# Optimization experiments

Measured on AMD Instinct MI355X. Metric: run time of the kernel, lower is better.

Reference implementation:

```python
import jax, jax.numpy as jnp
import numpy as np

D_MODEL = 1024
N_HEADS = 16
D_FF = 4096
HEAD_DIM = D_MODEL // N_HEADS
EPS = 1e-5


def setup_inputs() -> dict:
    key = jax.random.key(0)
    ks = jax.random.split(key, 12)
    B, S, D = 2, 2048, D_MODEL
    s = 0.02
    return {
        "x": jax.random.normal(ks[0], (B, S, D), jnp.float32),
        "ln1_g": jnp.ones((D,), jnp.float32),
        "ln1_b": jnp.zeros((D,), jnp.float32),
        "qkv_w": jax.random.normal(ks[1], (3 * D, D), jnp.float32) * s,
        "qkv_b": jnp.zeros((3 * D,), jnp.float32),
        "out_w": jax.random.normal(ks[2], (D, D), jnp.float32) * s,
        "out_b": jnp.zeros((D,), jnp.float32),
        "ln2_g": jnp.ones((D,), jnp.float32),
        "ln2_b": jnp.zeros((D,), jnp.float32),
        "fc1_w": jax.random.normal(ks[3], (D_FF, D), jnp.float32) * s,
        "fc1_b": jnp.zeros((D_FF,), jnp.float32),
        "fc2_w": jax.random.normal(ks[4], (D, D_FF), jnp.float32) * s,
        "fc2_b": jnp.zeros((D,), jnp.float32),
    }


def _layernorm(x, g, b):
    mu = jnp.mean(x, axis=-1, keepdims=True)
    var = jnp.mean(jnp.square(x - mu), axis=-1, keepdims=True)
    return (x - mu) * jax.lax.rsqrt(var + EPS) * g + b


def _attention(h, qkv_w, qkv_b, out_w, out_b):
    B, S, D = h.shape
    qkv = h @ qkv_w.T + qkv_b  # [B,S,3D]
    q, k, v = jnp.split(qkv, 3, axis=-1)
    # [B,H,S,hd]
    q = q.reshape(B, S, N_HEADS, HEAD_DIM).transpose(0, 2, 1, 3)
    k = k.reshape(B, S, N_HEADS, HEAD_DIM).transpose(0, 2, 1, 3)
    v = v.reshape(B, S, N_HEADS, HEAD_DIM).transpose(0, 2, 1, 3)
    scale = HEAD_DIM ** -0.5
    scores = jnp.einsum("bhqd,bhkd->bhqk", q, k) * scale
    causal = jnp.tril(jnp.ones((S, S), bool))
    scores = jnp.where(causal, scores, -jnp.inf)
    attn = jax.nn.softmax(scores, axis=-1)
    out = jnp.einsum("bhqk,bhkd->bhqd", attn, v)
    out = out.transpose(0, 2, 1, 3).reshape(B, S, D)
    return out @ out_w.T + out_b


def reference(x, ln1_g, ln1_b, qkv_w, qkv_b, out_w, out_b,
              ln2_g, ln2_b, fc1_w, fc1_b, fc2_w, fc2_b):
    x = x + _attention(_layernorm(x, ln1_g, ln1_b), qkv_w, qkv_b, out_w, out_b)
    h = _layernorm(x, ln2_g, ln2_b)
    ff = jax.nn.gelu(h @ fc1_w.T + fc1_b, approximate=False) @ fc2_w.T + fc2_b
    return x + ff
```

## Files before the change

### kernel.cpp

```cpp
#include <hip/hip_runtime.h>
#include <stdint.h>

typedef uint16_t u16;
typedef uint32_t u32;
typedef __bf16 bf16_t;
typedef bf16_t bf16x8 __attribute__((ext_vector_type(8)));
typedef float f32x4 __attribute__((ext_vector_type(4)));
typedef u16 u16x4 __attribute__((ext_vector_type(4)));
typedef u16 u16x8 __attribute__((ext_vector_type(8)));

__device__ __forceinline__ float bf2f(u16 v) {
    union { u32 u; float f; } x; x.u = ((u32)v) << 16; return x.f;
}
__device__ __forceinline__ u16 f2bf(float f) {
    union { float f; u32 u; } x; x.f = f;
    u32 r = (x.u + 0x7fffu + ((x.u >> 16) & 1u)) >> 16;
    return (u16)r;
}

__device__ __forceinline__ void gload_lds16(const u16* g, u16* l) {
    __builtin_amdgcn_global_load_lds(
        (const __attribute__((address_space(1))) void*)g,
        (__attribute__((address_space(3))) void*)l,
        16, 0, 0);
}
#define WAIT_ALL() __builtin_amdgcn_s_waitcnt(0)
#define WAITVM(n) __builtin_amdgcn_s_waitcnt(0x0F70 | (n))
#define BARRIER() __builtin_amdgcn_s_barrier()

__global__ __launch_bounds__(256) void cvt_kernel(
    const float* __restrict__ src, u16* __restrict__ dst, int n4)
{
    int i = blockIdx.x * 256 + threadIdx.x;
    if (i >= n4) return;
    f32x4 v = ((const f32x4*)src)[i];
    u16x4 o;
#pragma unroll
    for (int j = 0; j < 4; j++) o[j] = f2bf(v[j]);
    ((u16x4*)dst)[i] = o;
}

__global__ __launch_bounds__(256) void ln_kernel(
    const float* __restrict__ x, const float* __restrict__ g,
    const float* __restrict__ b, u16* __restrict__ out)
{
    const int row = blockIdx.x;
    const int tid = threadIdx.x;
    f32x4 xv = *(const f32x4*)(x + (size_t)row * 1024 + tid * 4);
    float v[4];
    float s = 0.f, s2 = 0.f;
#pragma unroll
    for (int i = 0; i < 4; i++) { v[i] = xv[i]; s += v[i]; s2 += v[i] * v[i]; }
#pragma unroll
    for (int off = 1; off < 64; off <<= 1) {
        s  += __shfl_xor(s, off);
        s2 += __shfl_xor(s2, off);
    }
    __shared__ float ws1[4], ws2[4];
    if ((tid & 63) == 0) { ws1[tid >> 6] = s; ws2[tid >> 6] = s2; }
    __syncthreads();
    s  = ws1[0] + ws1[1] + ws1[2] + ws1[3];
    s2 = ws2[0] + ws2[1] + ws2[2] + ws2[3];
    float mu  = s * (1.0f / 1024.0f);
    float var = s2 * (1.0f / 1024.0f) - mu * mu;
    float rstd = rsqrtf(var + 1e-5f);
    f32x4 gv = *(const f32x4*)(g + tid * 4);
    f32x4 bv = *(const f32x4*)(b + tid * 4);
    u16x4 ov;
#pragma unroll
    for (int i = 0; i < 4; i++)
        ov[i] = f2bf((v[i] - mu) * rstd * gv[i] + bv[i]);
    *(u16x4*)(out + (size_t)row * 1024 + tid * 4) = ov;
}

__global__ __launch_bounds__(256, 2) void gemm_bt(
    const u16* __restrict__ A, const u16* __restrict__ Bt,
    const float* __restrict__ bias, const float* res,
    void* C, int N, int K, int lda, int gelu)
{
    __shared__ __align__(16) u16 sA[2][128 * 32];
    __shared__ __align__(16) u16 sB[2][128 * 32];
    const int tid  = threadIdx.x;
    const int wave = tid >> 6, lane = tid & 63;
    const int lm = lane & 15, quad = lane >> 4;
    const int wm = wave >> 1, wn = wave & 1;
    const int row0 = blockIdx.y * 128, col0 = blockIdx.x * 128;
    const int r16 = lane >> 2;
    const int c8  = (lane & 3) * 8;
    const int niter = K >> 5;

    const u16* gsrc;
    size_t gstride;
    int chunk0;
    if (wave < 2) {
        chunk0 = wave * 4;
        gsrc = A + (size_t)(row0 + chunk0 * 16 + r16) * lda + c8;
        gstride = lda;
    } else {
        chunk0 = (wave - 2) * 4;
        gsrc = Bt + (size_t)(col0 + chunk0 * 16 + r16) * K + c8;
        gstride = K;
    }
    u16* lbase0 = (wave < 2) ? &sA[0][chunk0 * 512] : &sB[0][chunk0 * 512];
    u16* lbase1 = (wave < 2) ? &sA[1][chunk0 * 512] : &sB[1][chunk0 * 512];

    f32x4 acc[4][4];
#pragma unroll
    for (int i = 0; i < 4; i++)
#pragma unroll
        for (int j = 0; j < 4; j++) acc[i][j] = f32x4{0.f, 0.f, 0.f, 0.f};

#pragma unroll
    for (int j = 0; j < 4; j++)
        gload_lds16(gsrc + (size_t)(j * 16) * gstride, lbase0 + j * 512);

    for (int k = 0; k < niter; k++) {
        const int cur = k & 1;
        if (k + 1 < niter) {
            const u16* gs = gsrc + (size_t)(k + 1) * 32;
            u16* lb = cur ? lbase0 : lbase1;
#pragma unroll
            for (int j = 0; j < 4; j++)
                gload_lds16(gs + (size_t)(j * 16) * gstride, lb + j * 512);
            WAITVM(4);
        } else {
            WAITVM(0);
        }
        BARRIER();

        bf16x8 af[4], bfr[4];
#pragma unroll
        for (int t = 0; t < 4; t++)
            af[t] = *(const bf16x8*)&sA[cur][(wm * 64 + t * 16 + lm) * 32 + quad * 8];
#pragma unroll
        for (int t = 0; t < 4; t++)
            bfr[t] = *(const bf16x8*)&sB[cur][(wn * 64 + t * 16 + lm) * 32 + quad * 8];
#pragma unroll
        for (int i = 0; i < 4; i++)
#pragma unroll
            for (int j = 0; j < 4; j++)
                acc[i][j] = __builtin_amdgcn_mfma_f32_16x16x32_bf16(af[i], bfr[j], acc[i][j], 0, 0, 0);

        BARRIER();
    }

    float bj[4];
#pragma unroll
    for (int j = 0; j < 4; j++) bj[j] = bias[col0 + wn * 64 + j * 16 + lm];
#pragma unroll
    for (int i = 0; i < 4; i++) {
        int rbase = row0 + wm * 64 + i * 16 + quad * 4;
#pragma unroll
        for (int j = 0; j < 4; j++) {
            int c = col0 + wn * 64 + j * 16 + lm;
#pragma unroll
            for (int r = 0; r < 4; r++) {
                float v = acc[i][j][r] + bj[j];
                if (gelu) v = 0.5f * v * (1.0f + erff(v * 0.70710678118f));
                size_t idx = (size_t)(rbase + r) * N + c;
                if (res) {
                    ((float*)C)[idx] = v + res[idx];
                } else {
                    ((u16*)C)[idx] = f2bf(v);
                }
            }
        }
    }
}

__global__ __launch_bounds__(256, 2) void gemm_bt64(
    const u16* __restrict__ A, const u16* __restrict__ Bt,
    const float* __restrict__ bias, const float* res,
    void* C, int N, int K, int lda, int gelu)
{
    __shared__ __align__(16) u16 sA[2][128 * 32];
    __shared__ __align__(16) u16 sB[2][64 * 32];
    const int tid  = threadIdx.x;
    const int wave = tid >> 6, lane = tid & 63;
    const int lm = lane & 15, quad = lane >> 4;
    const int wm = wave >> 1, wn = wave & 1;
    const int row0 = blockIdx.y * 128, col0 = blockIdx.x * 64;
    const int r16 = lane >> 2;
    const int c8  = (lane & 3) * 8;
    const int niter = K >> 5;

    const u16* gs_[3];
    u16* lb0_[3];
    u16* lb1_[3];
    size_t gstride_[3];
#pragma unroll
    for (int j = 0; j < 3; j++) {
        int cid = wave * 3 + j;
        if (cid < 8) {
            gs_[j] = A + (size_t)(row0 + cid * 16 + r16) * lda + c8;
            gstride_[j] = lda;
            lb0_[j] = &sA[0][cid * 512];
            lb1_[j] = &sA[1][cid * 512];
        } else {
            int bc = cid - 8;
            gs_[j] = Bt + (size_t)(col0 + bc * 16 + r16) * K + c8;
            gstride_[j] = K;
            lb0_[j] = &sB[0][bc * 512];
            lb1_[j] = &sB[1][bc * 512];
        }
    }

    f32x4 acc[4][2];
#pragma unroll
    for (int i = 0; i < 4; i++)
#pragma unroll
        for (int j = 0; j < 2; j++) acc[i][j] = f32x4{0.f, 0.f, 0.f, 0.f};

#pragma unroll
    for (int j = 0; j < 3; j++) gload_lds16(gs_[j], lb0_[j]);

    for (int k = 0; k < niter; k++) {
        const int cur = k & 1;
        if (k + 1 < niter) {
#pragma unroll
            for (int j = 0; j < 3; j++)
                gload_lds16(gs_[j] + (size_t)(k + 1) * 32, cur ? lb0_[j] : lb1_[j]);
            WAITVM(3);
        } else {
            WAITVM(0);
        }
        BARRIER();

        bf16x8 af[4], bfr[2];
#pragma unroll
        for (int t = 0; t < 4; t++)
            af[t] = *(const bf16x8*)&sA[cur][(wm * 64 + t * 16 + lm) * 32 + quad * 8];
#pragma unroll
        for (int t = 0; t < 2; t++)
            bfr[t] = *(const bf16x8*)&sB[cur][(wn * 32 + t * 16 + lm) * 32 + quad * 8];
#pragma unroll
        for (int i = 0; i < 4; i++)
#pragma unroll
            for (int j = 0; j < 2; j++)
                acc[i][j] = __builtin_amdgcn_mfma_f32_16x16x32_bf16(af[i], bfr[j], acc[i][j], 0, 0, 0);

        BARRIER();
    }

    float bj[2];
#pragma unroll
    for (int j = 0; j < 2; j++) bj[j] = bias[col0 + wn * 32 + j * 16 + lm];
#pragma unroll
    for (int i = 0; i < 4; i++) {
        int rbase = row0 + wm * 64 + i * 16 + quad * 4;
#pragma unroll
        for (int j = 0; j < 2; j++) {
            int c = col0 + wn * 32 + j * 16 + lm;
#pragma unroll
            for (int r = 0; r < 4; r++) {
                float v = acc[i][j][r] + bj[j];
                if (gelu) v = 0.5f * v * (1.0f + erff(v * 0.70710678118f));
                size_t idx = (size_t)(rbase + r) * N + c;
                if (res) {
                    ((float*)C)[idx] = v + res[idx];
                } else {
                    ((u16*)C)[idx] = f2bf(v);
                }
            }
        }
    }
}

__global__ __launch_bounds__(256, 4) void attn_kernel(u16* qkv)
{
    __shared__ __align__(16) u16 sQ[64 * 64];
    __shared__ __align__(16) u16 sK[64 * 64];
    __shared__ __align__(16) u16 sVT[64 * 64];
    __shared__ __align__(16) u16 sP[4 * 16 * 72];

    const int tid  = threadIdx.x;
    const int wave = tid >> 6, lane = tid & 63;
    const int lm = lane & 15, quad = lane >> 4;
    int xi = blockIdx.x;
    int qz = (xi & 1) ? (31 - (xi >> 1)) : (xi >> 1);
    int qi = ((blockIdx.y >> 3) & 1) ? (31 - qz) : qz;
    const int q0 = qi * 64;
    const int b = blockIdx.y >> 4, h = blockIdx.y & 15;
    const size_t tok0 = (size_t)b * 2048;
    const int qcol = h * 64, kcol = 1024 + h * 64, vcol = 2048 + h * 64;
    const int r8 = lane >> 3;
    const int c8 = (lane & 7) * 8;

#pragma unroll
    for (int j = 0; j < 2; j++) {
        int chunk = wave * 2 + j;
        int r = chunk * 8 + r8;
        gload_lds16(qkv + (tok0 + q0 + r) * 3072 + qcol + c8, &sQ[chunk * 512]);
    }
    WAIT_ALL();
    __syncthreads();

    bf16x8 aq[2];
#pragma unroll
    for (int kk = 0; kk < 2; kk++)
        aq[kk] = *(const bf16x8*)&sQ[(wave * 16 + lm) * 64 + kk * 32 + quad * 8];

    f32x4 oacc[4];
    float mrun[4], lrun[4];
#pragma unroll
    for (int n = 0; n < 4; n++) oacc[n] = f32x4{0.f, 0.f, 0.f, 0.f};
#pragma unroll
    for (int r = 0; r < 4; r++) { mrun[r] = -1e30f; lrun[r] = 0.f; }

    const int vkey = tid >> 2;
    const int vdq  = (tid & 3) * 16;
    const int vpos = (((vkey >> 3) ^ (tid & 3)) << 3) | (vkey & 7);

    u16* sPw = &sP[wave * 16 * 72];
    const int ntiles = qi + 1;

    for (int tk = 0; tk < ntiles; tk++) {
        const int kb = tk * 64;
        __syncthreads();
#pragma unroll
        for (int j = 0; j < 2; j++) {
            int chunk = wave * 2 + j;
            int r = chunk * 8 + r8;
            gload_lds16(qkv + (tok0 + kb + r) * 3072 + kcol + c8, &sK[chunk * 512]);
        }
        {
            const u16* vr = qkv + (tok0 + kb + vkey) * 3072 + vcol + vdq;
            u16x8 v0 = *(const u16x8*)vr;
            u16x8 v1 = *(const u16x8*)(vr + 8);
#pragma unroll
            for (int i = 0; i < 8; i++) sVT[(vdq + i) * 64 + vpos] = v0[i];
#pragma unroll
            for (int i = 0; i < 8; i++) sVT[(vdq + 8 + i) * 64 + vpos] = v1[i];
        }
        WAIT_ALL();
        __syncthreads();

        float sc[4][4];
#pragma unroll
        for (int n = 0; n < 4; n++) {
            f32x4 s = f32x4{0.f, 0.f, 0.f, 0.f};
#pragma unroll
            for (int kk = 0; kk < 2; kk++) {
                bf16x8 bk = *(const bf16x8*)&sK[(n * 16 + lm) * 64 + kk * 32 + quad * 8];
                s = __builtin_amdgcn_mfma_f32_16x16x32_bf16(aq[kk], bk, s, 0, 0, 0);
            }
            int col  = kb + n * 16 + lm;
            int rowb = q0 + wave * 16 + quad * 4;
#pragma unroll
            for (int r = 0; r < 4; r++)
                sc[n][r] = (col <= rowb + r) ? s[r] * 0.125f : -1e30f;
        }
#pragma unroll
        for (int r = 0; r < 4; r++) {
            float mx = fmaxf(fmaxf(sc[0][r], sc[1][r]), fmaxf(sc[2][r], sc[3][r]));
#pragma unroll
            for (int off = 1; off < 16; off <<= 1) mx = fmaxf(mx, __shfl_xor(mx, off));
            float mnew  = fmaxf(mrun[r], mx);
            float alpha = __expf(mrun[r] - mnew);
            float sum = 0.f;
#pragma unroll
            for (int n = 0; n < 4; n++) {
                float p = __expf(sc[n][r] - mnew);
                sc[n][r] = p;
                sum += p;
            }
#pragma unroll
            for (int off = 1; off < 16; off <<= 1) sum += __shfl_xor(sum, off);
            lrun[r] = lrun[r] * alpha + sum;
            mrun[r] = mnew;
#pragma unroll
            for (int n = 0; n < 4; n++) oacc[n][r] *= alpha;
        }
#pragma unroll
        for (int n = 0; n < 4; n++)
#pragma unroll
            for (int r = 0; r < 4; r++)
                sPw[(quad * 4 + r) * 72 + n * 16 + lm] = f2bf(sc[n][r]);
        bf16x8 ap[2];
#pragma unroll
        for (int kk = 0; kk < 2; kk++)
            ap[kk] = *(const bf16x8*)&sPw[lm * 72 + kk * 32 + quad * 8];
#pragma unroll
        for (int n = 0; n < 4; n++)
#pragma unroll
            for (int kk = 0; kk < 2; kk++) {
                bf16x8 bv = *(const bf16x8*)
                    &sVT[(n * 16 + lm) * 64 + (((kk * 4 + quad) ^ n) << 3)];
                oacc[n] = __builtin_amdgcn_mfma_f32_16x16x32_bf16(ap[kk], bv, oacc[n], 0, 0, 0);
            }
    }

    {
        int rowb = q0 + wave * 16 + quad * 4;
#pragma unroll
        for (int r = 0; r < 4; r++) {
            float inv = 1.0f / lrun[r];
#pragma unroll
            for (int n = 0; n < 4; n++) {
                int d = n * 16 + lm;
                qkv[(tok0 + rowb + r) * 3072 + qcol + d] = f2bf(oacc[n][r] * inv);
            }
        }
    }
}

extern "C" void kernel_launch(void* const* d_in, const int* in_sizes, int n_in,
                              void* d_out, int out_size, void* d_ws, size_t ws_size,
                              hipStream_t stream)
{
    (void)in_sizes; (void)n_in; (void)out_size; (void)ws_size;
    const float* x    = (const float*)d_in[0];
    const float* ln1g = (const float*)d_in[1];
    const float* ln1b = (const float*)d_in[2];
    const float* qkvwF= (const float*)d_in[3];
    const float* qkvb = (const float*)d_in[4];
    const float* outwF= (const float*)d_in[5];
    const float* outb = (const float*)d_in[6];
    const float* ln2g = (const float*)d_in[7];
    const float* ln2b = (const float*)d_in[8];
    const float* fc1wF= (const float*)d_in[9];
    const float* fc1b = (const float*)d_in[10];
    const float* fc2wF= (const float*)d_in[11];
    const float* fc2b = (const float*)d_in[12];
    float* out = (float*)d_out;
    u16*   ws  = (u16*)d_ws;
    const int M1 = 1 << 20;

    u16* qkvw = ws;
    u16* outw = ws + 3 * M1;
    u16* qkvB = ws + 4 * M1;
    u16* ff1  = ws;
    u16* fc1w = ws + 16 * M1;
    u16* fc2w = ws + 20 * M1;
    u16* h    = ws + 24 * M1;

    cvt_kernel<<<3072, 256, 0, stream>>>(qkvwF, qkvw, 3 * M1 / 4);
    cvt_kernel<<<1024, 256, 0, stream>>>(outwF, outw, 1 * M1 / 4);
    cvt_kernel<<<4096, 256, 0, stream>>>(fc1wF, fc1w, 4 * M1 / 4);
    cvt_kernel<<<4096, 256, 0, stream>>>(fc2wF, fc2w, 4 * M1 / 4);

    ln_kernel<<<4096, 256, 0, stream>>>(x, ln1g, ln1b, h);
    gemm_bt<<<dim3(24, 32), 256, 0, stream>>>(h, qkvw, qkvb, nullptr, qkvB,
                                              3072, 1024, 1024, 0);
    attn_kernel<<<dim3(32, 32), 256, 0, stream>>>(qkvB);
    gemm_bt64<<<dim3(16, 32), 256, 0, stream>>>(qkvB, outw, outb, x, out,
                                                1024, 1024, 3072, 0);
    ln_kernel<<<4096, 256, 0, stream>>>(out, ln2g, ln2b, h);
    gemm_bt<<<dim3(32, 32), 256, 0, stream>>>(h, fc1w, fc1b, nullptr, ff1,
                                              4096, 1024, 1024, 1);
    gemm_bt64<<<dim3(16, 32), 256, 0, stream>>>(ff1, fc2w, fc2b, out, out,
                                                1024, 4096, 4096, 0);
}
```

Before: 401.8 us.

## Double-buffer K/V tiles in attention, swizzle LDS, merge weight conversions

The attention kernel now double-buffers K and transposed-V tiles in LDS, prefetching the next tile's K via async global-to-LDS loads and V into registers while the current tile is computed. Q/K/V LDS layouts get an XOR swizzle to reduce bank conflicts. The four weight-conversion launches are merged into a single kernel to cut launch overhead. The doubled LDS footprint lowers the occupancy hint from 4 to 3 blocks per CU, and the loop adds an extra barrier per tile.

```diff
diff --git a/kernel.cpp b/kernel.cpp
--- a/kernel.cpp
+++ b/kernel.cpp
@@ -26,18 +26,26 @@
 }
 #define WAIT_ALL() __builtin_amdgcn_s_waitcnt(0)
 #define WAITVM(n) __builtin_amdgcn_s_waitcnt(0x0F70 | (n))
+#define WAIT_LGKM0() __builtin_amdgcn_s_waitcnt(0xC07F)
 #define BARRIER() __builtin_amdgcn_s_barrier()
 
-__global__ __launch_bounds__(256) void cvt_kernel(
-    const float* __restrict__ src, u16* __restrict__ dst, int n4)
+__global__ __launch_bounds__(256) void cvt4_kernel(
+    const float* __restrict__ s0, const float* __restrict__ s1,
+    const float* __restrict__ s2, const float* __restrict__ s3,
+    u16* __restrict__ d0, u16* __restrict__ d1,
+    u16* __restrict__ d2, u16* __restrict__ d3)
 {
     int i = blockIdx.x * 256 + threadIdx.x;
-    if (i >= n4) return;
-    f32x4 v = ((const f32x4*)src)[i];
+    const float* s; u16* d; int off;
+    if (i < 786432)       { s = s0; d = d0; off = i; }
+    else if (i < 1048576) { s = s1; d = d1; off = i - 786432; }
+    else if (i < 2097152) { s = s2; d = d2; off = i - 1048576; }
+    else                  { s = s3; d = d3; off = i - 2097152; }
+    f32x4 v = ((const f32x4*)s)[off];
     u16x4 o;
 #pragma unroll
     for (int j = 0; j < 4; j++) o[j] = f2bf(v[j]);
-    ((u16x4*)dst)[i] = o;
+    ((u16x4*)d)[off] = o;
 }
 
 __global__ __launch_bounds__(256) void ln_kernel(
@@ -187,23 +195,22 @@
     const u16* gs_[3];
     u16* lb0_[3];
     u16* lb1_[3];
-    size_t gstride_[3];
 #pragma unroll
     for (int j = 0; j < 3; j++) {
         int cid = wave * 3 + j;
         if (cid < 8) {
             gs_[j] = A + (size_t)(row0 + cid * 16 + r16) * lda + c8;
-            gstride_[j] = lda;
             lb0_[j] = &sA[0][cid * 512];
             lb1_[j] = &sA[1][cid * 512];
         } else {
             int bc = cid - 8;
             gs_[j] = Bt + (size_t)(col0 + bc * 16 + r16) * K + c8;
-            gstride_[j] = K;
             lb0_[j] = &sB[0][bc * 512];
             lb1_[j] = &sB[1][bc * 512];
         }
     }
+    const size_t gstride_a = lda, gstride_b = K;
+    (void)gstride_a; (void)gstride_b;
 
     f32x4 acc[4][2];
 #pragma unroll
@@ -266,11 +273,11 @@
     }
 }
 
-__global__ __launch_bounds__(256, 4) void attn_kernel(u16* qkv)
+__global__ __launch_bounds__(256, 3) void attn_kernel(u16* qkv)
 {
     __shared__ __align__(16) u16 sQ[64 * 64];
-    __shared__ __align__(16) u16 sK[64 * 64];
-    __shared__ __align__(16) u16 sVT[64 * 64];
+    __shared__ __align__(16) u16 sK[2][64 * 64];
+    __shared__ __align__(16) u16 sVT[2][64 * 64];
     __shared__ __align__(16) u16 sP[4 * 16 * 72];
 
     const int tid  = threadIdx.x;
@@ -284,21 +291,35 @@
     const size_t tok0 = (size_t)b * 2048;
     const int qcol = h * 64, kcol = 1024 + h * 64, vcol = 2048 + h * 64;
     const int r8 = lane >> 3;
-    const int c8 = (lane & 7) * 8;
+    const int c8s = (((lane & 7) ^ r8) << 3);
+
+    const int vkey = tid >> 2;
+    const int vq   = tid & 3;
+    const int vdq  = vq * 16;
+    const u16* vbase = qkv + (tok0 + vkey) * 3072 + vcol + vdq;
 
 #pragma unroll
     for (int j = 0; j < 2; j++) {
         int chunk = wave * 2 + j;
         int r = chunk * 8 + r8;
-        gload_lds16(qkv + (tok0 + q0 + r) * 3072 + qcol + c8, &sQ[chunk * 512]);
-    }
-    WAIT_ALL();
-    __syncthreads();
+        gload_lds16(qkv + (tok0 + q0 + r) * 3072 + qcol + c8s, &sQ[chunk * 512]);
+    }
+#pragma unroll
+    for (int j = 0; j < 2; j++) {
+        int chunk = wave * 2 + j;
+        int r = chunk * 8 + r8;
+        gload_lds16(qkv + (tok0 + r) * 3072 + kcol + c8s, &sK[0][chunk * 512]);
+    }
+    u16x8 va = *(const u16x8*)vbase;
+    u16x8 vb = *(const u16x8*)(vbase + 8);
+    WAITVM(4);
+    BARRIER();
 
     bf16x8 aq[2];
 #pragma unroll
     for (int kk = 0; kk < 2; kk++)
-        aq[kk] = *(const bf16x8*)&sQ[(wave * 16 + lm) * 64 + kk * 32 + quad * 8];
+        aq[kk] = *(const bf16x8*)
+            &sQ[(wave * 16 + lm) * 64 + (((kk * 4 + quad) ^ (lm & 7)) << 3)];
 
     f32x4 oacc[4];
     float mrun[4], lrun[4];
@@ -307,41 +328,51 @@
 #pragma unroll
     for (int r = 0; r < 4; r++) { mrun[r] = -1e30f; lrun[r] = 0.f; }
 
-    const int vkey = tid >> 2;
-    const int vdq  = (tid & 3) * 16;
-    const int vpos = (((vkey >> 3) ^ (tid & 3)) << 3) | (vkey & 7);
-
     u16* sPw = &sP[wave * 16 * 72];
     const int ntiles = qi + 1;
 
     for (int tk = 0; tk < ntiles; tk++) {
+        const int cur = tk & 1;
+        u16x8 na = va, nb = vb;
+        if (tk + 1 < ntiles) {
+            const int kb1 = (tk + 1) * 64;
+#pragma unroll
+            for (int j = 0; j < 2; j++) {
+                int chunk = wave * 2 + j;
+                int r = chunk * 8 + r8;
+                gload_lds16(qkv + (tok0 + kb1 + r) * 3072 + kcol + c8s,
+                            &sK[1 - cur][chunk * 512]);
+            }
+            const u16* vr = vbase + (size_t)kb1 * 3072;
+            na = *(const u16x8*)vr;
+            nb = *(const u16x8*)(vr + 8);
+            WAITVM(4);
+        } else {
+            WAITVM(0);
+        }
+#pragma unroll
+        for (int i = 0; i < 8; i++) {
+            int d = vdq + i;
+            sVT[cur][d * 64 + ((((vkey >> 3) ^ i ^ vq)) << 3) + (vkey & 7)] = va[i];
+        }
+#pragma unroll
+        for (int i = 0; i < 8; i++) {
+            int d = vdq + 8 + i;
+            sVT[cur][d * 64 + ((((vkey >> 3) ^ i ^ vq)) << 3) + (vkey & 7)] = vb[i];
+        }
+        va = na; vb = nb;
+        WAIT_LGKM0();
+        BARRIER();
+
         const int kb = tk * 64;
-        __syncthreads();
-#pragma unroll
-        for (int j = 0; j < 2; j++) {
-            int chunk = wave * 2 + j;
-            int r = chunk * 8 + r8;
-            gload_lds16(qkv + (tok0 + kb + r) * 3072 + kcol + c8, &sK[chunk * 512]);
-        }
-        {
-            const u16* vr = qkv + (tok0 + kb + vkey) * 3072 + vcol + vdq;
-            u16x8 v0 = *(const u16x8*)vr;
-            u16x8 v1 = *(const u16x8*)(vr + 8);
-#pragma unroll
-            for (int i = 0; i < 8; i++) sVT[(vdq + i) * 64 + vpos] = v0[i];
-#pragma unroll
-            for (int i = 0; i < 8; i++) sVT[(vdq + 8 + i) * 64 + vpos] = v1[i];
-        }
-        WAIT_ALL();
-        __syncthreads();
-
         float sc[4][4];
 #pragma unroll
         for (int n = 0; n < 4; n++) {
             f32x4 s = f32x4{0.f, 0.f, 0.f, 0.f};
 #pragma unroll
             for (int kk = 0; kk < 2; kk++) {
-                bf16x8 bk = *(const bf16x8*)&sK[(n * 16 + lm) * 64 + kk * 32 + quad * 8];
+                bf16x8 bk = *(const bf16x8*)
+                    &sK[cur][(n * 16 + lm) * 64 + (((kk * 4 + quad) ^ (lm & 7)) << 3)];
                 s = __builtin_amdgcn_mfma_f32_16x16x32_bf16(aq[kk], bk, s, 0, 0, 0);
             }
             int col  = kb + n * 16 + lm;
@@ -385,9 +416,12 @@
 #pragma unroll
             for (int kk = 0; kk < 2; kk++) {
                 bf16x8 bv = *(const bf16x8*)
-                    &sVT[(n * 16 + lm) * 64 + (((kk * 4 + quad) ^ n) << 3)];
+                    &sVT[cur][(n * 16 + lm) * 64 +
+                              ((((kk * 4 + quad) ^ (lm & 7) ^ n)) << 3)];
                 oacc[n] = __builtin_amdgcn_mfma_f32_16x16x32_bf16(ap[kk], bv, oacc[n], 0, 0, 0);
             }
+
+        BARRIER();
     }
 
     {
@@ -434,10 +468,8 @@
     u16* fc2w = ws + 20 * M1;
     u16* h    = ws + 24 * M1;
 
-    cvt_kernel<<<3072, 256, 0, stream>>>(qkvwF, qkvw, 3 * M1 / 4);
-    cvt_kernel<<<1024, 256, 0, stream>>>(outwF, outw, 1 * M1 / 4);
-    cvt_kernel<<<4096, 256, 0, stream>>>(fc1wF, fc1w, 4 * M1 / 4);
-    cvt_kernel<<<4096, 256, 0, stream>>>(fc2wF, fc2w, 4 * M1 / 4);
+    cvt4_kernel<<<12288, 256, 0, stream>>>(qkvwF, outwF, fc1wF, fc2wF,
+                                           qkvw, outw, fc1w, fc2w);
 
     ln_kernel<<<4096, 256, 0, stream>>>(x, ln1g, ln1b, h);
     gemm_bt<<<dim3(24, 32), 256, 0, stream>>>(h, qkvw, qkvb, nullptr, qkvB,
```

Result: no change. 405.0 us (+0.8%).
